# Kernel tuning notes

Measured on AMD Instinct MI355X. Metric: run time of the kernel, lower is better.

Reference implementation:

```python
import jax, jax.numpy as jnp
import numpy as np

N_NODES = 100000
N_HE = 25000
N_CONN = 400000
D = 256
L = 2
MEAN_EPS = 1e-8   # matches torch code's hyperedge-size epsilon
LN_EPS = 1e-5     # torch LayerNorm default
LRELU_SLOPE = 0.2


def setup_inputs() -> dict:
    key = jax.random.key(0)
    ks = jax.random.split(key, 6)
    s = 1.0 / np.sqrt(D).astype(np.float32)
    return {
        "x": jax.random.normal(ks[0], (N_NODES, D), jnp.float32),
        "node_W": jax.random.normal(ks[1], (L, D, D), jnp.float32) * s,
        "node_b": jnp.zeros((L, D), jnp.float32),
        "he_W": jax.random.normal(ks[2], (L, D, D), jnp.float32) * s,
        "he_b": jnp.zeros((L, D), jnp.float32),
        "ln_g": jnp.ones((L, D), jnp.float32),
        "ln_b": jnp.zeros((L, D), jnp.float32),
        "hyperedge_weight": jax.random.uniform(ks[3], (N_HE,), jnp.float32) + 0.5,
        "node_idx": jax.random.randint(ks[4], (N_CONN,), 0, N_NODES, jnp.int64),
        "he_idx": jax.random.randint(ks[5], (N_CONN,), 0, N_HE, jnp.int64),
    }


def _hg_conv(x, Wn, bn, We, be, g, b, w, node_idx, he_idx, n_he):
    # x: [N, D] node features
    xt = x @ Wn + bn                                   # node_transform
    ones = jnp.ones((node_idx.shape[0],), xt.dtype)
    # nodes -> hyperedges (scatter-mean with +eps as in torch code)
    he_sum = jax.ops.segment_sum(xt[node_idx], he_idx, num_segments=n_he)
    he_cnt = jax.ops.segment_sum(ones, he_idx, num_segments=n_he)
    he = he_sum / (he_cnt[:, None] + MEAN_EPS)
    he = (he @ We + be) * w[:, None]                   # hyperedge_transform + weight
    # hyperedges -> nodes (gather then scatter_mean; zero for isolated nodes)
    n_sum = jax.ops.segment_sum(he[he_idx], node_idx, num_segments=x.shape[0])
    n_cnt = jax.ops.segment_sum(ones, node_idx, num_segments=x.shape[0])
    agg = jnp.where(n_cnt[:, None] > 0, n_sum / jnp.maximum(n_cnt, 1.0)[:, None], 0.0)
    # residual + layernorm + leaky relu (dropout is identity at eval)
    h = agg + xt
    mu = jnp.mean(h, axis=-1, keepdims=True)
    var = jnp.var(h, axis=-1, keepdims=True)
    h = (h - mu) * jax.lax.rsqrt(var + LN_EPS) * g + b
    return jax.nn.leaky_relu(h, LRELU_SLOPE)


def reference(x, node_W, node_b, he_W, he_b, ln_g, ln_b, hyperedge_weight, node_idx, he_idx):
    n_he = hyperedge_weight.shape[0]
    n_layers = node_W.shape[0]
    for i in range(n_layers):
        res = x
        x = _hg_conv(x, node_W[i], node_b[i], he_W[i], he_b[i],
                     ln_g[i], ln_b[i], hyperedge_weight, node_idx, he_idx, n_he)
        if i > 0:
            x = x + res
    return x
```

## Files before the change

### kernel.cpp

```cpp
#include <hip/hip_runtime.h>

#define D 256
#define N_NODES 100000
#define N_HE 25000
#define N_CONN 400000

constexpr float MEAN_EPS = 1e-8f;
constexpr float LN_EPS   = 1e-5f;
constexpr float SLOPE    = 0.2f;

typedef __attribute__((ext_vector_type(8))) short short8;
typedef __attribute__((ext_vector_type(4))) float f32x4;
typedef __attribute__((ext_vector_type(16))) float f32x16;
typedef __attribute__((ext_vector_type(4))) unsigned short ushort4v;

static __device__ __forceinline__ unsigned short f2bf(float f) {
  unsigned int u = __builtin_bit_cast(unsigned int, f);
  u = (u + 0x7FFFu + ((u >> 16) & 1u)) >> 16;
  return (unsigned short)u;
}
static __device__ __forceinline__ float bf2f(unsigned short u) {
  return __builtin_bit_cast(float, (unsigned int)u << 16);
}

__global__ __launch_bounds__(256) void hist_kernel(
    const int* __restrict__ node_idx, const int* __restrict__ he_idx,
    int* __restrict__ he_deg, int* __restrict__ n_deg) {
  int c = blockIdx.x * 256 + threadIdx.x;
  if (c < N_CONN) {
    atomicAdd(&he_deg[he_idx[c]], 1);
    atomicAdd(&n_deg[node_idx[c]], 1);
  }
}

__global__ __launch_bounds__(256) void alloc_kernel(
    const int* __restrict__ he_deg, const int* __restrict__ n_deg,
    int* __restrict__ totals,
    int* __restrict__ he_start, int* __restrict__ he_cur,
    int* __restrict__ n_start, int* __restrict__ n_cur) {
  int i = blockIdx.x * 256 + threadIdx.x;
  if (i < N_HE) {
    int s = atomicAdd(&totals[0], he_deg[i]);
    he_start[i] = s;
    he_cur[i] = s;
  }
  if (i < N_NODES) {
    int s = atomicAdd(&totals[1], n_deg[i]);
    n_start[i] = s;
    n_cur[i] = s;
  }
}

__global__ __launch_bounds__(256) void fill_kernel(
    const int* __restrict__ node_idx, const int* __restrict__ he_idx,
    int* __restrict__ he_cur, int* __restrict__ n_cur,
    int* __restrict__ he_list, int* __restrict__ n_list) {
  int c = blockIdx.x * 256 + threadIdx.x;
  if (c < N_CONN) {
    int n = node_idx[c];
    int e = he_idx[c];
    int p = atomicAdd(&he_cur[e], 1);
    he_list[p] = n;
    int q = atomicAdd(&n_cur[n], 1);
    n_list[q] = e;
  }
}

__global__ __launch_bounds__(256) void convert_w(
    const float* __restrict__ W, unsigned short* __restrict__ Wt) {
  int m = blockIdx.x >> 4;
  int tile = blockIdx.x & 15;
  int k0 = (tile >> 2) * 64, n0 = (tile & 3) * 64;
  const float* Win = W + (size_t)m * 65536;
  unsigned short* Wout = Wt + (size_t)m * 65536;
  __shared__ unsigned short T[64][65];
  int t = threadIdx.x;
  int r = t >> 6, c = t & 63;
  #pragma unroll 4
  for (int i = 0; i < 16; ++i) {
    int kr = i * 4 + r;
    T[kr][c] = f2bf(Win[(size_t)(k0 + kr) * 256 + n0 + c]);
  }
  __syncthreads();
  #pragma unroll 4
  for (int i = 0; i < 16; ++i) {
    int nr = i * 4 + r;
    Wout[(size_t)(n0 + nr) * 256 + k0 + c] = T[c][nr];
  }
}

template <int A_F32, int O_F32>
__global__ __launch_bounds__(512, 4) void gemm32(
    const void* __restrict__ Ain, const unsigned short* __restrict__ Wt,
    const float* __restrict__ bias, const float* __restrict__ hw,
    void* __restrict__ outv, int M) {
  __shared__ unsigned short As[64 * 256];
  const int t = threadIdx.x;
  const int wave = t >> 6, lane = t & 63;
  const int l31 = lane & 31, lhi = lane >> 5;
  const int colbase = wave * 32;
  const int row0 = blockIdx.x * 64;

  f32x4 B[16];
  {
    const unsigned short* bp = Wt + (size_t)(colbase + l31) * 256 + lhi * 8;
    #pragma unroll
    for (int kc = 0; kc < 16; ++kc)
      B[kc] = *(const f32x4*)(bp + kc * 16);
  }
  #pragma unroll
  for (int kc = 0; kc < 16; ++kc)
    asm volatile("" : "+v"(B[kc]));

  float biasv = bias[colbase + l31];

  if (A_F32) {
    const float* A = (const float*)Ain;
    #pragma unroll
    for (int i = 0; i < 8; ++i) {
      int row = i * 8 + (t >> 6);
      int col4 = t & 63;
      int r = row0 + row;
      float4 v = (r < M) ? ((const float4*)(A + (size_t)r * D))[col4]
                         : make_float4(0.f, 0.f, 0.f, 0.f);
      ushort4v o;
      o[0] = f2bf(v.x); o[1] = f2bf(v.y); o[2] = f2bf(v.z); o[3] = f2bf(v.w);
      unsigned int byte = (unsigned)(row * 512 + col4 * 8) ^ (unsigned)((row & 7) << 4);
      *(ushort4v*)((char*)As + byte) = o;
    }
  } else {
    const unsigned short* A = (const unsigned short*)Ain;
    #pragma unroll
    for (int i = 0; i < 4; ++i) {
      int row = i * 16 + (t >> 5);
      int e = t & 31;
      int r = row0 + row;
      short8 v = {};
      if (r < M) v = *(const short8*)(A + (size_t)r * D + e * 8);
      unsigned int byte = (unsigned)(row * 512 + e * 16) ^ (unsigned)((row & 7) << 4);
      *(short8*)((char*)As + byte) = v;
    }
  }
  __syncthreads();

  f32x16 acc0 = (f32x16)0.f, acc1 = (f32x16)0.f;
  #pragma unroll
  for (int kc = 0; kc < 16; ++kc) {
    int r0 = l31;
    unsigned int ad0 = (unsigned)(r0 * 512 + kc * 32 + lhi * 16) ^ (unsigned)((r0 & 7) << 4);
    short8 a0 = *(const short8*)((const char*)As + ad0);
    int r1 = 32 + l31;
    unsigned int ad1 = (unsigned)(r1 * 512 + kc * 32 + lhi * 16) ^ (unsigned)((r1 & 7) << 4);
    short8 a1 = *(const short8*)((const char*)As + ad1);
    short8 b = __builtin_bit_cast(short8, B[kc]);
    acc0 = __builtin_amdgcn_mfma_f32_32x32x16_bf16(a0, b, acc0, 0, 0, 0);
    acc1 = __builtin_amdgcn_mfma_f32_32x32x16_bf16(a1, b, acc1, 0, 0, 0);
  }

  const int col = colbase + l31;
  #pragma unroll
  for (int rt = 0; rt < 2; ++rt) {
    #pragma unroll
    for (int reg = 0; reg < 16; ++reg) {
      int row = (reg & 3) + 8 * (reg >> 2) + 4 * lhi;
      int grow = row0 + rt * 32 + row;
      if (grow < M) {
        float wv = hw ? hw[grow] : 1.f;
        float v = ((rt == 0) ? acc0[reg] : acc1[reg]) + biasv;
        v *= wv;
        if (O_F32) {
          ((float*)outv)[(size_t)grow * D + col] = v;
        } else {
          ((unsigned short*)outv)[(size_t)grow * D + col] = f2bf(v);
        }
      }
    }
  }
}

__global__ __launch_bounds__(256) void gather_he_kernel(
    const unsigned short* __restrict__ xt, const int* __restrict__ he_start,
    const int* __restrict__ he_deg, const int* __restrict__ he_list,
    unsigned short* __restrict__ he_out) {
  int e = blockIdx.x * 4 + (threadIdx.x >> 6);
  if (e >= N_HE) return;
  int lane = threadIdx.x & 63;
  int s = he_start[e];
  int deg = he_deg[e];

  float a0 = 0.f, a1 = 0.f, a2 = 0.f, a3 = 0.f;
  int i = 0;
  for (; i + 4 <= deg; i += 4) {
    int n0 = he_list[s + i + 0];
    int n1 = he_list[s + i + 1];
    int n2 = he_list[s + i + 2];
    int n3 = he_list[s + i + 3];
    ushort4v v0 = ((const ushort4v*)(xt + (size_t)n0 * D))[lane];
    ushort4v v1 = ((const ushort4v*)(xt + (size_t)n1 * D))[lane];
    ushort4v v2 = ((const ushort4v*)(xt + (size_t)n2 * D))[lane];
    ushort4v v3 = ((const ushort4v*)(xt + (size_t)n3 * D))[lane];
    a0 += bf2f(v0[0]) + bf2f(v1[0]) + bf2f(v2[0]) + bf2f(v3[0]);
    a1 += bf2f(v0[1]) + bf2f(v1[1]) + bf2f(v2[1]) + bf2f(v3[1]);
    a2 += bf2f(v0[2]) + bf2f(v1[2]) + bf2f(v2[2]) + bf2f(v3[2]);
    a3 += bf2f(v0[3]) + bf2f(v1[3]) + bf2f(v2[3]) + bf2f(v3[3]);
  }
  for (; i < deg; ++i) {
    int n = he_list[s + i];
    ushort4v v = ((const ushort4v*)(xt + (size_t)n * D))[lane];
    a0 += bf2f(v[0]); a1 += bf2f(v[1]); a2 += bf2f(v[2]); a3 += bf2f(v[3]);
  }
  float inv = 1.0f / ((float)deg + MEAN_EPS);
  ushort4v o;
  o[0] = f2bf(a0 * inv); o[1] = f2bf(a1 * inv);
  o[2] = f2bf(a2 * inv); o[3] = f2bf(a3 * inv);
  ((ushort4v*)(he_out + (size_t)e * D))[lane] = o;
}

__global__ __launch_bounds__(256) void gather_node_finalize(
    const unsigned short* __restrict__ he_feat, const int* __restrict__ n_start,
    const int* __restrict__ n_deg, const int* __restrict__ n_list,
    const unsigned short* __restrict__ xt, const float* __restrict__ g,
    const float* __restrict__ b, const float* __restrict__ res,
    float* __restrict__ out, int add_res) {
  int node = blockIdx.x * 4 + (threadIdx.x >> 6);
  if (node >= N_NODES) return;
  int lane = threadIdx.x & 63;
  int s = n_start[node];
  int deg = n_deg[node];

  float a0 = 0.f, a1 = 0.f, a2 = 0.f, a3 = 0.f;
  int i = 0;
  for (; i + 4 <= deg; i += 4) {
    int e0 = n_list[s + i + 0];
    int e1 = n_list[s + i + 1];
    int e2 = n_list[s + i + 2];
    int e3 = n_list[s + i + 3];
    ushort4v v0 = ((const ushort4v*)(he_feat + (size_t)e0 * D))[lane];
    ushort4v v1 = ((const ushort4v*)(he_feat + (size_t)e1 * D))[lane];
    ushort4v v2 = ((const ushort4v*)(he_feat + (size_t)e2 * D))[lane];
    ushort4v v3 = ((const ushort4v*)(he_feat + (size_t)e3 * D))[lane];
    a0 += bf2f(v0[0]) + bf2f(v1[0]) + bf2f(v2[0]) + bf2f(v3[0]);
    a1 += bf2f(v0[1]) + bf2f(v1[1]) + bf2f(v2[1]) + bf2f(v3[1]);
    a2 += bf2f(v0[2]) + bf2f(v1[2]) + bf2f(v2[2]) + bf2f(v3[2]);
    a3 += bf2f(v0[3]) + bf2f(v1[3]) + bf2f(v2[3]) + bf2f(v3[3]);
  }
  for (; i < deg; ++i) {
    int e = n_list[s + i];
    ushort4v v = ((const ushort4v*)(he_feat + (size_t)e * D))[lane];
    a0 += bf2f(v[0]); a1 += bf2f(v[1]); a2 += bf2f(v[2]); a3 += bf2f(v[3]);
  }
  float inv = deg > 0 ? 1.0f / (float)deg : 0.0f;

  ushort4v xv = ((const ushort4v*)(xt + (size_t)node * D))[lane];
  float h0 = a0 * inv + bf2f(xv[0]);
  float h1 = a1 * inv + bf2f(xv[1]);
  float h2 = a2 * inv + bf2f(xv[2]);
  float h3 = a3 * inv + bf2f(xv[3]);

  float sum = h0 + h1 + h2 + h3;
  float ss  = h0 * h0 + h1 * h1 + h2 * h2 + h3 * h3;
  #pragma unroll
  for (int o = 32; o > 0; o >>= 1) {
    sum += __shfl_xor(sum, o, 64);
    ss  += __shfl_xor(ss, o, 64);
  }
  float mu  = sum * (1.0f / D);
  float var = ss * (1.0f / D) - mu * mu;
  float rstd = rsqrtf(var + LN_EPS);

  float4 gv = ((const float4*)g)[lane];
  float4 bv = ((const float4*)b)[lane];

  float o0 = (h0 - mu) * rstd * gv.x + bv.x;
  float o1 = (h1 - mu) * rstd * gv.y + bv.y;
  float o2 = (h2 - mu) * rstd * gv.z + bv.z;
  float o3 = (h3 - mu) * rstd * gv.w + bv.w;
  o0 = o0 >= 0.f ? o0 : o0 * SLOPE;
  o1 = o1 >= 0.f ? o1 : o1 * SLOPE;
  o2 = o2 >= 0.f ? o2 : o2 * SLOPE;
  o3 = o3 >= 0.f ? o3 : o3 * SLOPE;

  if (add_res) {
    float4 rv = ((const float4*)(res + (size_t)node * D))[lane];
    o0 += rv.x; o1 += rv.y; o2 += rv.z; o3 += rv.w;
  }

  ((float4*)(out + (size_t)node * D))[lane] = make_float4(o0, o1, o2, o3);
}

extern "C" void kernel_launch(void* const* d_in, const int* in_sizes, int n_in,
                              void* d_out, int out_size, void* d_ws, size_t ws_size,
                              hipStream_t stream) {
  const float* x       = (const float*)d_in[0];
  const float* node_W  = (const float*)d_in[1];
  const float* node_b  = (const float*)d_in[2];
  const float* he_W    = (const float*)d_in[3];
  const float* he_b    = (const float*)d_in[4];
  const float* ln_g    = (const float*)d_in[5];
  const float* ln_b    = (const float*)d_in[6];
  const float* hw      = (const float*)d_in[7];
  const int*   node_idx = (const int*)d_in[8];
  const int*   he_idx   = (const int*)d_in[9];
  float* out = (float*)d_out;

  unsigned short* xt     = (unsigned short*)d_ws;
  unsigned short* he_buf = xt + (size_t)N_NODES * D;
  unsigned short* Wt_node = he_buf + (size_t)N_HE * D;
  unsigned short* Wt_he   = Wt_node + 2 * 65536;
  int* he_deg   = (int*)(Wt_he + 2 * 65536);
  int* n_deg    = he_deg + N_HE;
  int* totals   = n_deg + N_NODES;
  int* he_start = totals + 2;
  int* he_cur   = he_start + N_HE;
  int* n_start  = he_cur + N_HE;
  int* n_cur    = n_start + N_NODES;
  int* he_list  = n_cur + N_NODES;
  int* n_list   = he_list + N_CONN;

  convert_w<<<32, 256, 0, stream>>>(node_W, Wt_node);
  convert_w<<<32, 256, 0, stream>>>(he_W, Wt_he);

  hipMemsetAsync(he_deg, 0, (size_t)(N_HE + N_NODES + 2) * sizeof(int), stream);
  hist_kernel<<<(N_CONN + 255) / 256, 256, 0, stream>>>(node_idx, he_idx, he_deg, n_deg);
  alloc_kernel<<<(N_NODES + 255) / 256, 256, 0, stream>>>(
      he_deg, n_deg, totals, he_start, he_cur, n_start, n_cur);
  fill_kernel<<<(N_CONN + 255) / 256, 256, 0, stream>>>(
      node_idx, he_idx, he_cur, n_cur, he_list, n_list);

  const int ntiles_node = (N_NODES + 63) / 64;
  const int ntiles_he   = (N_HE + 63) / 64;

  for (int l = 0; l < 2; ++l) {
    const float* xin = (l == 0) ? x : out;
    const float* bn = node_b + (size_t)l * D;
    const float* be = he_b + (size_t)l * D;
    const float* g  = ln_g + (size_t)l * D;
    const float* bb = ln_b + (size_t)l * D;

    gemm32<1, 0><<<ntiles_node, 512, 0, stream>>>(
        xin, Wt_node + (size_t)l * 65536, bn, nullptr, xt, N_NODES);
    gather_he_kernel<<<(N_HE + 3) / 4, 256, 0, stream>>>(
        xt, he_start, he_deg, he_list, he_buf);
    gemm32<0, 0><<<ntiles_he, 512, 0, stream>>>(
        he_buf, Wt_he + (size_t)l * 65536, be, hw, he_buf, N_HE);
    gather_node_finalize<<<(N_NODES + 3) / 4, 256, 0, stream>>>(
        he_buf, n_start, n_deg, n_list, xt, g, bb, xin, out, l);
  }
}
```

Measured before the change: 464.3 us.

## Fuse hyperedge gather with GEMM, pipeline node GEMM, store layer-1 output as bf16

The hyperedge mean-gather now writes straight into LDS and feeds the hyperedge GEMM in one kernel, so the bf16 hyperedge buffer no longer makes a global round trip. The node GEMM becomes a persistent kernel with 512 blocks that prefetch the next tile into registers and double-buffer the A tile in LDS. The layer-0 output is stored as bf16 rather than fp32, cutting bytes for the layer-1 GEMM input and residual read. The two weight conversions merge into one launch. The bf16 intermediate adds rounding error to the residual path, and the fused hyperedge kernel has only 391 blocks doing serial per-wave gathers.

```diff
diff --git a/kernel.cpp b/kernel.cpp
--- a/kernel.cpp
+++ b/kernel.cpp
@@ -67,11 +67,13 @@
 }
 
 __global__ __launch_bounds__(256) void convert_w(
-    const float* __restrict__ W, unsigned short* __restrict__ Wt) {
+    const float* __restrict__ Wnode, const float* __restrict__ Whe,
+    unsigned short* __restrict__ Wt) {
   int m = blockIdx.x >> 4;
   int tile = blockIdx.x & 15;
   int k0 = (tile >> 2) * 64, n0 = (tile & 3) * 64;
-  const float* Win = W + (size_t)m * 65536;
+  const float* Win = (m < 2) ? (Wnode + (size_t)m * 65536)
+                             : (Whe + (size_t)(m - 2) * 65536);
   unsigned short* Wout = Wt + (size_t)m * 65536;
   __shared__ unsigned short T[64][65];
   int t = threadIdx.x;
@@ -89,17 +91,16 @@
   }
 }
 
-template <int A_F32, int O_F32>
-__global__ __launch_bounds__(512, 4) void gemm32(
+template <int A_F32>
+__global__ __launch_bounds__(512, 4) void gemm_node_pipe(
     const void* __restrict__ Ain, const unsigned short* __restrict__ Wt,
-    const float* __restrict__ bias, const float* __restrict__ hw,
-    void* __restrict__ outv, int M) {
-  __shared__ unsigned short As[64 * 256];
+    const float* __restrict__ bias, unsigned short* __restrict__ out,
+    int M, int ntiles) {
+  __shared__ unsigned short As[2][64 * 256];
   const int t = threadIdx.x;
   const int wave = t >> 6, lane = t & 63;
   const int l31 = lane & 31, lhi = lane >> 5;
   const int colbase = wave * 32;
-  const int row0 = blockIdx.x * 64;
 
   f32x4 B[16];
   {
@@ -111,46 +112,207 @@
   #pragma unroll
   for (int kc = 0; kc < 16; ++kc)
     asm volatile("" : "+v"(B[kc]));
-
   float biasv = bias[colbase + l31];
 
-  if (A_F32) {
-    const float* A = (const float*)Ain;
+  float4 sregf[8];
+  short8 sregb[4];
+
+  {
+    const int row0 = blockIdx.x * 64;
+    if (A_F32) {
+      const float* A = (const float*)Ain;
+      #pragma unroll
+      for (int i = 0; i < 8; ++i) {
+        int row = i * 8 + (t >> 6);
+        int c4 = t & 63;
+        int r = row0 + row;
+        sregf[i] = (r < M) ? ((const float4*)(A + (size_t)r * D))[c4]
+                           : make_float4(0.f, 0.f, 0.f, 0.f);
+      }
+      #pragma unroll
+      for (int i = 0; i < 8; ++i) {
+        int row = i * 8 + (t >> 6);
+        int c4 = t & 63;
+        ushort4v o;
+        o[0] = f2bf(sregf[i].x); o[1] = f2bf(sregf[i].y);
+        o[2] = f2bf(sregf[i].z); o[3] = f2bf(sregf[i].w);
+        unsigned int byte = (unsigned)(row * 512 + c4 * 8) ^ (unsigned)((row & 7) << 4);
+        *(ushort4v*)((char*)As[0] + byte) = o;
+      }
+    } else {
+      const unsigned short* A = (const unsigned short*)Ain;
+      #pragma unroll
+      for (int i = 0; i < 4; ++i) {
+        int row = i * 16 + (t >> 5);
+        int e = t & 31;
+        int r = row0 + row;
+        short8 v = {};
+        if (r < M) v = *(const short8*)(A + (size_t)r * D + e * 8);
+        sregb[i] = v;
+      }
+      #pragma unroll
+      for (int i = 0; i < 4; ++i) {
+        int row = i * 16 + (t >> 5);
+        int e = t & 31;
+        unsigned int byte = (unsigned)(row * 512 + e * 16) ^ (unsigned)((row & 7) << 4);
+        *(short8*)((char*)As[0] + byte) = sregb[i];
+      }
+    }
+  }
+
+  int cur = 0;
+  for (int tile = blockIdx.x; tile < ntiles; tile += gridDim.x) {
+    const int next = tile + gridDim.x;
+    __syncthreads();
+
+    if (next < ntiles) {
+      const int nrow0 = next * 64;
+      if (A_F32) {
+        const float* A = (const float*)Ain;
+        #pragma unroll
+        for (int i = 0; i < 8; ++i) {
+          int row = i * 8 + (t >> 6);
+          int c4 = t & 63;
+          int r = nrow0 + row;
+          sregf[i] = (r < M) ? ((const float4*)(A + (size_t)r * D))[c4]
+                             : make_float4(0.f, 0.f, 0.f, 0.f);
+        }
+      } else {
+        const unsigned short* A = (const unsigned short*)Ain;
+        #pragma unroll
+        for (int i = 0; i < 4; ++i) {
+          int row = i * 16 + (t >> 5);
+          int e = t & 31;
+          int r = nrow0 + row;
+          short8 v = {};
+          if (r < M) v = *(const short8*)(A + (size_t)r * D + e * 8);
+          sregb[i] = v;
+        }
+      }
+    }
+
+    const int row0 = tile * 64;
+    const char* Ab = (const char*)As[cur];
+    f32x16 acc0 = (f32x16)0.f, acc1 = (f32x16)0.f;
     #pragma unroll
-    for (int i = 0; i < 8; ++i) {
-      int row = i * 8 + (t >> 6);
-      int col4 = t & 63;
-      int r = row0 + row;
-      float4 v = (r < M) ? ((const float4*)(A + (size_t)r * D))[col4]
-                         : make_float4(0.f, 0.f, 0.f, 0.f);
-      ushort4v o;
-      o[0] = f2bf(v.x); o[1] = f2bf(v.y); o[2] = f2bf(v.z); o[3] = f2bf(v.w);
-      unsigned int byte = (unsigned)(row * 512 + col4 * 8) ^ (unsigned)((row & 7) << 4);
-      *(ushort4v*)((char*)As + byte) = o;
-    }
-  } else {
-    const unsigned short* A = (const unsigned short*)Ain;
+    for (int kc = 0; kc < 16; ++kc) {
+      unsigned int ad0 = (unsigned)(l31 * 512 + kc * 32 + lhi * 16) ^ (unsigned)((l31 & 7) << 4);
+      short8 a0 = *(const short8*)(Ab + ad0);
+      unsigned int ad1 = (unsigned)((32 + l31) * 512 + kc * 32 + lhi * 16) ^ (unsigned)((l31 & 7) << 4);
+      short8 a1 = *(const short8*)(Ab + ad1);
+      short8 b = __builtin_bit_cast(short8, B[kc]);
+      acc0 = __builtin_amdgcn_mfma_f32_32x32x16_bf16(a0, b, acc0, 0, 0, 0);
+      acc1 = __builtin_amdgcn_mfma_f32_32x32x16_bf16(a1, b, acc1, 0, 0, 0);
+    }
+
+    const int col = colbase + l31;
     #pragma unroll
-    for (int i = 0; i < 4; ++i) {
-      int row = i * 16 + (t >> 5);
-      int e = t & 31;
-      int r = row0 + row;
-      short8 v = {};
-      if (r < M) v = *(const short8*)(A + (size_t)r * D + e * 8);
-      unsigned int byte = (unsigned)(row * 512 + e * 16) ^ (unsigned)((row & 7) << 4);
-      *(short8*)((char*)As + byte) = v;
-    }
+    for (int rt = 0; rt < 2; ++rt) {
+      #pragma unroll
+      for (int reg = 0; reg < 16; ++reg) {
+        int row = (reg & 3) + 8 * (reg >> 2) + 4 * lhi;
+        int grow = row0 + rt * 32 + row;
+        if (grow < M) {
+          float v = ((rt == 0) ? acc0[reg] : acc1[reg]) + biasv;
+          out[(size_t)grow * D + col] = f2bf(v);
+        }
+      }
+    }
+
+    if (next < ntiles) {
+      if (A_F32) {
+        #pragma unroll
+        for (int i = 0; i < 8; ++i) {
+          int row = i * 8 + (t >> 6);
+          int c4 = t & 63;
+          ushort4v o;
+          o[0] = f2bf(sregf[i].x); o[1] = f2bf(sregf[i].y);
+          o[2] = f2bf(sregf[i].z); o[3] = f2bf(sregf[i].w);
+          unsigned int byte = (unsigned)(row * 512 + c4 * 8) ^ (unsigned)((row & 7) << 4);
+          *(ushort4v*)((char*)As[cur ^ 1] + byte) = o;
+        }
+      } else {
+        #pragma unroll
+        for (int i = 0; i < 4; ++i) {
+          int row = i * 16 + (t >> 5);
+          int e = t & 31;
+          unsigned int byte = (unsigned)(row * 512 + e * 16) ^ (unsigned)((row & 7) << 4);
+          *(short8*)((char*)As[cur ^ 1] + byte) = sregb[i];
+        }
+      }
+    }
+    cur ^= 1;
+  }
+}
+
+__global__ __launch_bounds__(512, 4) void he_fused(
+    const unsigned short* __restrict__ xt, const int* __restrict__ he_start,
+    const int* __restrict__ he_deg, const int* __restrict__ he_list,
+    const unsigned short* __restrict__ Wt, const float* __restrict__ bias,
+    const float* __restrict__ hwp, unsigned short* __restrict__ he_out) {
+  __shared__ unsigned short As[64 * 256];
+  const int t = threadIdx.x;
+  const int wave = t >> 6, lane = t & 63;
+  const int l31 = lane & 31, lhi = lane >> 5;
+  const int colbase = wave * 32;
+
+  f32x4 B[16];
+  {
+    const unsigned short* bp = Wt + (size_t)(colbase + l31) * 256 + lhi * 8;
+    #pragma unroll
+    for (int kc = 0; kc < 16; ++kc)
+      B[kc] = *(const f32x4*)(bp + kc * 16);
+  }
+  #pragma unroll
+  for (int kc = 0; kc < 16; ++kc)
+    asm volatile("" : "+v"(B[kc]));
+  float biasv = bias[colbase + l31];
+
+  const int e0 = blockIdx.x * 64;
+  for (int j = 0; j < 8; ++j) {
+    int row = wave * 8 + j;
+    int e = e0 + row;
+    float a0 = 0.f, a1 = 0.f, a2 = 0.f, a3 = 0.f;
+    float invv = 0.f;
+    if (e < N_HE) {
+      int s = he_start[e];
+      int deg = he_deg[e];
+      int i = 0;
+      for (; i + 4 <= deg; i += 4) {
+        int n0 = he_list[s + i + 0];
+        int n1 = he_list[s + i + 1];
+        int n2 = he_list[s + i + 2];
+        int n3 = he_list[s + i + 3];
+        ushort4v v0 = ((const ushort4v*)(xt + (size_t)n0 * D))[lane];
+        ushort4v v1 = ((const ushort4v*)(xt + (size_t)n1 * D))[lane];
+        ushort4v v2 = ((const ushort4v*)(xt + (size_t)n2 * D))[lane];
+        ushort4v v3 = ((const ushort4v*)(xt + (size_t)n3 * D))[lane];
+        a0 += bf2f(v0[0]) + bf2f(v1[0]) + bf2f(v2[0]) + bf2f(v3[0]);
+        a1 += bf2f(v0[1]) + bf2f(v1[1]) + bf2f(v2[1]) + bf2f(v3[1]);
+        a2 += bf2f(v0[2]) + bf2f(v1[2]) + bf2f(v2[2]) + bf2f(v3[2]);
+        a3 += bf2f(v0[3]) + bf2f(v1[3]) + bf2f(v2[3]) + bf2f(v3[3]);
+      }
+      for (; i < deg; ++i) {
+        int n = he_list[s + i];
+        ushort4v v = ((const ushort4v*)(xt + (size_t)n * D))[lane];
+        a0 += bf2f(v[0]); a1 += bf2f(v[1]); a2 += bf2f(v[2]); a3 += bf2f(v[3]);
+      }
+      invv = 1.0f / ((float)deg + MEAN_EPS);
+    }
+    ushort4v o;
+    o[0] = f2bf(a0 * invv); o[1] = f2bf(a1 * invv);
+    o[2] = f2bf(a2 * invv); o[3] = f2bf(a3 * invv);
+    unsigned int byte = (unsigned)(row * 512 + lane * 8) ^ (unsigned)((row & 7) << 4);
+    *(ushort4v*)((char*)As + byte) = o;
   }
   __syncthreads();
 
   f32x16 acc0 = (f32x16)0.f, acc1 = (f32x16)0.f;
   #pragma unroll
   for (int kc = 0; kc < 16; ++kc) {
-    int r0 = l31;
-    unsigned int ad0 = (unsigned)(r0 * 512 + kc * 32 + lhi * 16) ^ (unsigned)((r0 & 7) << 4);
+    unsigned int ad0 = (unsigned)(l31 * 512 + kc * 32 + lhi * 16) ^ (unsigned)((l31 & 7) << 4);
     short8 a0 = *(const short8*)((const char*)As + ad0);
-    int r1 = 32 + l31;
-    unsigned int ad1 = (unsigned)(r1 * 512 + kc * 32 + lhi * 16) ^ (unsigned)((r1 & 7) << 4);
+    unsigned int ad1 = (unsigned)((32 + l31) * 512 + kc * 32 + lhi * 16) ^ (unsigned)((l31 & 7) << 4);
     short8 a1 = *(const short8*)((const char*)As + ad1);
     short8 b = __builtin_bit_cast(short8, B[kc]);
     acc0 = __builtin_amdgcn_mfma_f32_32x32x16_bf16(a0, b, acc0, 0, 0, 0);
@@ -163,65 +325,22 @@
     #pragma unroll
     for (int reg = 0; reg < 16; ++reg) {
       int row = (reg & 3) + 8 * (reg >> 2) + 4 * lhi;
-      int grow = row0 + rt * 32 + row;
-      if (grow < M) {
-        float wv = hw ? hw[grow] : 1.f;
-        float v = ((rt == 0) ? acc0[reg] : acc1[reg]) + biasv;
-        v *= wv;
-        if (O_F32) {
-          ((float*)outv)[(size_t)grow * D + col] = v;
-        } else {
-          ((unsigned short*)outv)[(size_t)grow * D + col] = f2bf(v);
-        }
-      }
-    }
-  }
-}
-
-__global__ __launch_bounds__(256) void gather_he_kernel(
-    const unsigned short* __restrict__ xt, const int* __restrict__ he_start,
-    const int* __restrict__ he_deg, const int* __restrict__ he_list,
-    unsigned short* __restrict__ he_out) {
-  int e = blockIdx.x * 4 + (threadIdx.x >> 6);
-  if (e >= N_HE) return;
-  int lane = threadIdx.x & 63;
-  int s = he_start[e];
-  int deg = he_deg[e];
-
-  float a0 = 0.f, a1 = 0.f, a2 = 0.f, a3 = 0.f;
-  int i = 0;
-  for (; i + 4 <= deg; i += 4) {
-    int n0 = he_list[s + i + 0];
-    int n1 = he_list[s + i + 1];
-    int n2 = he_list[s + i + 2];
-    int n3 = he_list[s + i + 3];
-    ushort4v v0 = ((const ushort4v*)(xt + (size_t)n0 * D))[lane];
-    ushort4v v1 = ((const ushort4v*)(xt + (size_t)n1 * D))[lane];
-    ushort4v v2 = ((const ushort4v*)(xt + (size_t)n2 * D))[lane];
-    ushort4v v3 = ((const ushort4v*)(xt + (size_t)n3 * D))[lane];
-    a0 += bf2f(v0[0]) + bf2f(v1[0]) + bf2f(v2[0]) + bf2f(v3[0]);
-    a1 += bf2f(v0[1]) + bf2f(v1[1]) + bf2f(v2[1]) + bf2f(v3[1]);
-    a2 += bf2f(v0[2]) + bf2f(v1[2]) + bf2f(v2[2]) + bf2f(v3[2]);
-    a3 += bf2f(v0[3]) + bf2f(v1[3]) + bf2f(v2[3]) + bf2f(v3[3]);
-  }
-  for (; i < deg; ++i) {
-    int n = he_list[s + i];
-    ushort4v v = ((const ushort4v*)(xt + (size_t)n * D))[lane];
-    a0 += bf2f(v[0]); a1 += bf2f(v[1]); a2 += bf2f(v[2]); a3 += bf2f(v[3]);
-  }
-  float inv = 1.0f / ((float)deg + MEAN_EPS);
-  ushort4v o;
-  o[0] = f2bf(a0 * inv); o[1] = f2bf(a1 * inv);
-  o[2] = f2bf(a2 * inv); o[3] = f2bf(a3 * inv);
-  ((ushort4v*)(he_out + (size_t)e * D))[lane] = o;
-}
-
-__global__ __launch_bounds__(256) void gather_node_finalize(
+      int grow = e0 + rt * 32 + row;
+      if (grow < N_HE) {
+        float v = (((rt == 0) ? acc0[reg] : acc1[reg]) + biasv) * hwp[grow];
+        he_out[(size_t)grow * D + col] = f2bf(v);
+      }
+    }
+  }
+}
+
+template <int O_F32>
+__global__ __launch_bounds__(256) void finalize_k(
     const unsigned short* __restrict__ he_feat, const int* __restrict__ n_start,
     const int* __restrict__ n_deg, const int* __restrict__ n_list,
     const unsigned short* __restrict__ xt, const float* __restrict__ g,
-    const float* __restrict__ b, const float* __restrict__ res,
-    float* __restrict__ out, int add_res) {
+    const float* __restrict__ b, const unsigned short* __restrict__ res,
+    void* __restrict__ outv, int add_res) {
   int node = blockIdx.x * 4 + (threadIdx.x >> 6);
   if (node >= N_NODES) return;
   int lane = threadIdx.x & 63;
@@ -281,11 +400,17 @@
   o3 = o3 >= 0.f ? o3 : o3 * SLOPE;
 
   if (add_res) {
-    float4 rv = ((const float4*)(res + (size_t)node * D))[lane];
-    o0 += rv.x; o1 += rv.y; o2 += rv.z; o3 += rv.w;
-  }
-
-  ((float4*)(out + (size_t)node * D))[lane] = make_float4(o0, o1, o2, o3);
+    ushort4v rv = ((const ushort4v*)(res + (size_t)node * D))[lane];
+    o0 += bf2f(rv[0]); o1 += bf2f(rv[1]); o2 += bf2f(rv[2]); o3 += bf2f(rv[3]);
+  }
+
+  if (O_F32) {
+    ((float4*)((float*)outv + (size_t)node * D))[lane] = make_float4(o0, o1, o2, o3);
+  } else {
+    ushort4v ov;
+    ov[0] = f2bf(o0); ov[1] = f2bf(o1); ov[2] = f2bf(o2); ov[3] = f2bf(o3);
+    ((ushort4v*)((unsigned short*)outv + (size_t)node * D))[lane] = ov;
+  }
 }
 
 extern "C" void kernel_launch(void* const* d_in, const int* in_sizes, int n_in,
@@ -301,13 +426,12 @@
   const float* hw      = (const float*)d_in[7];
   const int*   node_idx = (const int*)d_in[8];
   const int*   he_idx   = (const int*)d_in[9];
-  float* out = (float*)d_out;
 
   unsigned short* xt     = (unsigned short*)d_ws;
   unsigned short* he_buf = xt + (size_t)N_NODES * D;
-  unsigned short* Wt_node = he_buf + (size_t)N_HE * D;
-  unsigned short* Wt_he   = Wt_node + 2 * 65536;
-  int* he_deg   = (int*)(Wt_he + 2 * 65536);
+  unsigned short* out_bf = he_buf + (size_t)N_HE * D;
+  unsigned short* Wt_all = out_bf + (size_t)N_NODES * D;
+  int* he_deg   = (int*)(Wt_all + 4 * 65536);
   int* n_deg    = he_deg + N_HE;
   int* totals   = n_deg + N_NODES;
   int* he_start = totals + 2;
@@ -317,8 +441,7 @@
   int* he_list  = n_cur + N_NODES;
   int* n_list   = he_list + N_CONN;
 
-  convert_w<<<32, 256, 0, stream>>>(node_W, Wt_node);
-  convert_w<<<32, 256, 0, stream>>>(he_W, Wt_he);
+  convert_w<<<64, 256, 0, stream>>>(node_W, he_W, Wt_all);
 
   hipMemsetAsync(he_deg, 0, (size_t)(N_HE + N_NODES + 2) * sizeof(int), stream);
   hist_kernel<<<(N_CONN + 255) / 256, 256, 0, stream>>>(node_idx, he_idx, he_deg, n_deg);
@@ -328,22 +451,31 @@
       node_idx, he_idx, he_cur, n_cur, he_list, n_list);
 
   const int ntiles_node = (N_NODES + 63) / 64;
-  const int ntiles_he   = (N_HE + 63) / 64;
+  const int nblk_he     = (N_HE + 63) / 64;
 
   for (int l = 0; l < 2; ++l) {
-    const float* xin = (l == 0) ? x : out;
+    const unsigned short* Wtn = Wt_all + (size_t)l * 65536;
+    const unsigned short* Wte = Wt_all + (size_t)(2 + l) * 65536;
     const float* bn = node_b + (size_t)l * D;
     const float* be = he_b + (size_t)l * D;
     const float* g  = ln_g + (size_t)l * D;
     const float* bb = ln_b + (size_t)l * D;
 
-    gemm32<1, 0><<<ntiles_node, 512, 0, stream>>>(
-        xin, Wt_node + (size_t)l * 65536, bn, nullptr, xt, N_NODES);
-    gather_he_kernel<<<(N_HE + 3) / 4, 256, 0, stream>>>(
-        xt, he_start, he_deg, he_list, he_buf);
-    gemm32<0, 0><<<ntiles_he, 512, 0, stream>>>(
-        he_buf, Wt_he + (size_t)l * 65536, be, hw, he_buf, N_HE);
-    gather_node_finalize<<<(N_NODES + 3) / 4, 256, 0, stream>>>(
-        he_buf, n_start, n_deg, n_list, xt, g, bb, xin, out, l);
-  }
-}
+    if (l == 0) {
+      gemm_node_pipe<1><<<512, 512, 0, stream>>>(
+          x, Wtn, bn, xt, N_NODES, ntiles_node);
+    } else {
+      gemm_node_pipe<0><<<512, 512, 0, stream>>>(
+          out_bf, Wtn, bn, xt, N_NODES, ntiles_node);
+    }
+    he_fused<<<nblk_he, 512, 0, stream>>>(
+        xt, he_start, he_deg, he_list, Wte, be, hw, he_buf);
+    if (l == 0) {
+      finalize_k<0><<<(N_NODES + 3) / 4, 256, 0, stream>>>(
+          he_buf, n_start, n_deg, n_list, xt, g, bb, nullptr, out_bf, 0);
+    } else {
+      finalize_k<1><<<(N_NODES + 3) / 4, 256, 0, stream>>>(
+          he_buf, n_start, n_deg, n_list, xt, g, bb, out_bf, d_out, 1);
+    }
+  }
+}
```

Measured after the change: 490.0 us. 1.06x slower.
